# Kernel tuning notes

Hardware: AMD Instinct MI355X
Metric: run time of the kernel (lower is better)

Reference implementation:

```python
import jax, jax.numpy as jnp
import numpy as np

B, N, C = 4, 2048, 768
H = 12
D = C // H  # head_dim = 64
SCALE = D ** -0.5


def setup_inputs() -> dict:
    key = jax.random.key(0)
    ks = jax.random.split(key, 9)
    x_q = jax.random.normal(ks[0], (B, N, C), dtype=jnp.float32)
    x_k = jax.random.normal(ks[1], (B, N, C), dtype=jnp.float32)
    x_v = jax.random.normal(ks[2], (B, N, C), dtype=jnp.float32)
    x_u = jax.random.uniform(ks[3], (B, N, C), dtype=jnp.float32)
    s = C ** -0.5
    Wq = jax.random.normal(ks[4], (C, C), dtype=jnp.float32) * s
    Wk = jax.random.normal(ks[5], (C, C), dtype=jnp.float32) * s
    Wv = jax.random.normal(ks[6], (C, C), dtype=jnp.float32) * s
    Wp = jax.random.normal(ks[7], (C, C), dtype=jnp.float32) * s
    bp = jax.random.normal(ks[8], (C,), dtype=jnp.float32) * 0.01
    return {"x_q": x_q, "x_k": x_k, "x_v": x_v, "x_u": x_u,
            "Wq": Wq, "Wk": Wk, "Wv": Wv, "Wp": Wp, "bp": bp}


def reference(x_q, x_k, x_v, x_u, Wq, Wk, Wv, Wp, bp):
    # Linear projections (torch Linear: y = x @ W.T), split into heads [B,H,N,D]
    def to_heads(x, W):
        y = jnp.einsum('bnc,oc->bno', x, W)
        return y.reshape(B, N, H, D).transpose(0, 2, 1, 3)
    q = to_heads(x_q, Wq) * SCALE
    k = to_heads(x_k, Wk)
    v = to_heads(x_v, Wv)
    # Scores [B,H,N,N]
    attn = jnp.einsum('bhqd,bhkd->bhqk', q, k)
    # Uncertainty map: per-query scalar (mean over channels), broadcast over keys & heads
    uc = jnp.mean(x_u, axis=-1)  # [B,N]
    attn = attn * uc[:, None, :, None]
    attn = jax.nn.softmax(attn, axis=-1)
    out = jnp.einsum('bhqk,bhkd->bhqd', attn, v)
    out = out.transpose(0, 2, 1, 3).reshape(B, N, C)
    return jnp.einsum('bnc,oc->bno', out, Wp) + bp
```

## Files before the change

kernel.cpp:

```cpp
#include <hip/hip_runtime.h>
#include <hip/hip_bf16.h>
#include <cstdint>

#define B_ 4
#define N_ 2048
#define C_ 768
#define H_ 12
#define D_ 64
#define QSCALE 0.18033688011112042f

typedef __bf16 bf16x8 __attribute__((ext_vector_type(8)));
typedef float f32x4 __attribute__((ext_vector_type(4)));

__device__ __forceinline__ unsigned f2bs(float x) {
  unsigned u = __builtin_bit_cast(unsigned, x);
  unsigned r = (u + 0x7fffu + ((u >> 16) & 1u)) >> 16;
  return r;
}

__device__ __forceinline__ bf16x8 ldb8(const unsigned short* p) {
  return __builtin_bit_cast(bf16x8, *(const uint4*)p);
}

__device__ __forceinline__ f32x4 mfma16(bf16x8 a, bf16x8 b, f32x4 c) {
  return __builtin_amdgcn_mfma_f32_16x16x32_bf16(a, b, c, 0, 0, 0);
}

__device__ __forceinline__ void async16(const unsigned short* g, unsigned short* l) {
  __builtin_amdgcn_global_load_lds(
      (const __attribute__((address_space(1))) unsigned int*)g,
      (__attribute__((address_space(3))) unsigned int*)l, 16, 0, 0);
}

__global__ void prep_kernel(
    const float* __restrict__ xq, const float* __restrict__ xk,
    const float* __restrict__ xv, const float* __restrict__ xu,
    const float* __restrict__ Wq, const float* __restrict__ Wk,
    const float* __restrict__ Wv, const float* __restrict__ Wp,
    unsigned short* __restrict__ dxq, unsigned short* __restrict__ dxk,
    unsigned short* __restrict__ dxv,
    unsigned short* __restrict__ dwq, unsigned short* __restrict__ dwk,
    unsigned short* __restrict__ dwv, unsigned short* __restrict__ dwp,
    float* __restrict__ uc) {
  const int id = blockIdx.x;
  if (id < 18432) {
    const float* s = (id < 6144) ? xq : (id < 12288) ? xk : xv;
    unsigned short* d = (id < 6144) ? dxq : (id < 12288) ? dxk : dxv;
    int i = ((id % 6144) * 256 + threadIdx.x) * 4;
    float4 v = *(const float4*)(s + i);
    ushort4 h;
    h.x = (unsigned short)f2bs(v.x); h.y = (unsigned short)f2bs(v.y);
    h.z = (unsigned short)f2bs(v.z); h.w = (unsigned short)f2bs(v.w);
    *(ushort4*)(d + i) = h;
  } else if (id < 20736) {
    int sub = id - 18432;
    int which = sub / 576;
    const float* s = (which == 0) ? Wq : (which == 1) ? Wk : (which == 2) ? Wv : Wp;
    unsigned short* d = (which == 0) ? dwq : (which == 1) ? dwk : (which == 2) ? dwv : dwp;
    int i = ((sub % 576) * 256 + threadIdx.x) * 4;
    float4 v = *(const float4*)(s + i);
    ushort4 h;
    h.x = (unsigned short)f2bs(v.x); h.y = (unsigned short)f2bs(v.y);
    h.z = (unsigned short)f2bs(v.z); h.w = (unsigned short)f2bs(v.w);
    *(ushort4*)(d + i) = h;
  } else {
    int sub = id - 20736;
    int w = threadIdx.x >> 6, lane = threadIdx.x & 63;
    int row = sub * 4 + w;
    const float* p = xu + (size_t)row * C_;
    float s = 0.f;
#pragma unroll
    for (int i = 0; i < 3; ++i) {
      float4 v = *(const float4*)(p + (i * 64 + lane) * 4);
      s += v.x + v.y + v.z + v.w;
    }
#pragma unroll
    for (int off = 1; off < 64; off <<= 1) s += __shfl_xor(s, off);
    if (lane == 0) uc[row] = s * (1.f / 768.f);
  }
}

__device__ __forceinline__ void gemm_mainloop(
    const unsigned short* __restrict__ A, const unsigned short* __restrict__ W,
    int m0, int n0, unsigned short* Al, unsigned short* Bl,
    int tid, int wm, int wn, int quad, int id15, f32x4 (*acc)[4]) {
  const int wb = tid & 192;
  const unsigned short* ap[4];
  const unsigned short* bp[4];
#pragma unroll
  for (int s = 0; s < 4; ++s) {
    int g = s * 256 + tid;
    int row = (g >> 2) & 127;
    int col = ((g >> 9) << 5) | ((g & 3) << 3);
    ap[s] = A + (size_t)(m0 + row) * C_ + col;
    bp[s] = W + (size_t)(n0 + row) * C_ + col;
  }

  for (int kt = 0; kt < C_; kt += 64) {
    __syncthreads();
#pragma unroll
    for (int s = 0; s < 4; ++s) {
      async16(ap[s] + kt, Al + (s * 256 + wb) * 8);
      async16(bp[s] + kt, Bl + (s * 256 + wb) * 8);
    }
    __syncthreads();

#pragma unroll
    for (int kk = 0; kk < 2; ++kk) {
      bf16x8 af[4], bfr[4];
#pragma unroll
      for (int i = 0; i < 4; ++i)
        af[i]  = ldb8(&Al[kk * 4096 + (wm + i * 16 + id15) * 32 + quad * 8]);
#pragma unroll
      for (int j = 0; j < 4; ++j)
        bfr[j] = ldb8(&Bl[kk * 4096 + (wn + j * 16 + id15) * 32 + quad * 8]);
#pragma unroll
      for (int i = 0; i < 4; ++i)
#pragma unroll
        for (int j = 0; j < 4; ++j)
          acc[i][j] = mfma16(af[i], bfr[j], acc[i][j]);
    }
  }
}

#define TSTR 136
__global__ __launch_bounds__(256, 3) void gemm_qkv(
    const unsigned short* __restrict__ xq, const unsigned short* __restrict__ xk,
    const unsigned short* __restrict__ xv,
    const unsigned short* __restrict__ wq, const unsigned short* __restrict__ wk,
    const unsigned short* __restrict__ wv,
    unsigned short* __restrict__ oq, unsigned short* __restrict__ ok,
    unsigned short* __restrict__ ov, const float* __restrict__ uc) {
  __shared__ __align__(16) unsigned short S[128 * TSTR];
  unsigned short* Al = S;
  unsigned short* Bl = S + 8192;
  const int tid = threadIdx.x;
  const int w = tid >> 6, lane = tid & 63, quad = lane >> 4, id15 = lane & 15;
  const int wm = (w >> 1) << 6, wn = (w & 1) << 6;
  const int id = blockIdx.x;
  const int xcd = id & 7, slot = id >> 3;
  const int n0 = (slot % 6) << 7;
  const int gz = xcd * 24 + slot / 6;
  const int z = gz >> 6, m0 = (gz & 63) << 7;

  const unsigned short* A = (z == 0) ? xq : (z == 1) ? xk : xv;
  const unsigned short* W = (z == 0) ? wq : (z == 1) ? wk : wv;

  f32x4 acc[4][4] = {};
  gemm_mainloop(A, W, m0, n0, Al, Bl, tid, wm, wn, quad, id15, acc);

  if (z == 2) {
    __syncthreads();
#pragma unroll
    for (int i = 0; i < 4; ++i)
#pragma unroll
      for (int j = 0; j < 4; ++j) {
        uint2 u;
        u.x = f2bs(acc[i][j][0]) | (f2bs(acc[i][j][1]) << 16);
        u.y = f2bs(acc[i][j][2]) | (f2bs(acc[i][j][3]) << 16);
        *(uint2*)&S[(wn + j * 16 + id15) * TSTR + wm + i * 16 + quad * 4] = u;
      }
    __syncthreads();
    const int b = m0 >> 11, nb = m0 & (N_ - 1);
#pragma unroll
    for (int s = 0; s < 8; ++s) {
      int c = s * 256 + tid;
      int row = c >> 4, o = (c & 15) << 3;
      *(uint4*)(ov + (size_t)(b * C_ + n0 + row) * N_ + nb + o) = *(const uint4*)&S[row * TSTR + o];
    }
    return;
  }

#pragma unroll
  for (int i = 0; i < 4; ++i) {
#pragma unroll
    for (int j = 0; j < 4; ++j) {
#pragma unroll
      for (int r = 0; r < 4; ++r) {
        int gm = m0 + wm + i * 16 + quad * 4 + r;
        int gn = n0 + wn + j * 16 + id15;
        float v = acc[i][j][r];
        if (z == 0) {
          v *= QSCALE * uc[gm];
          oq[(size_t)gm * C_ + gn] = (unsigned short)f2bs(v);
        } else {
          ok[(size_t)gm * C_ + gn] = (unsigned short)f2bs(v);
        }
      }
    }
  }
}

__global__ __launch_bounds__(256, 4) void gemm_out(
    const unsigned short* __restrict__ ao, const unsigned short* __restrict__ wp,
    float* __restrict__ out, const float* __restrict__ bias) {
  __shared__ __align__(16) unsigned short Al[64 * 64];
  __shared__ __align__(16) unsigned short Bl[128 * 64];
  const int tid = threadIdx.x;
  const int w = tid >> 6, lane = tid & 63, quad = lane >> 4, id15 = lane & 15;
  const int wm = (w >> 1) << 5, wn = (w & 1) << 6;
  const int id = blockIdx.x;
  const int xcd = id & 7, slot = id >> 3;
  const int n0 = (slot % 6) << 7;
  const int m0 = (xcd * 16 + slot / 6) << 6;

  const int wb = tid & 192;
  const unsigned short* ap[2];
#pragma unroll
  for (int s = 0; s < 2; ++s) {
    int g = s * 256 + tid;
    int row = (g >> 2) & 63;
    int col = ((g >> 8) << 5) | ((g & 3) << 3);
    ap[s] = ao + (size_t)(m0 + row) * C_ + col;
  }
  const unsigned short* bp[4];
#pragma unroll
  for (int s = 0; s < 4; ++s) {
    int g = s * 256 + tid;
    int row = (g >> 2) & 127;
    int col = ((g >> 9) << 5) | ((g & 3) << 3);
    bp[s] = wp + (size_t)(n0 + row) * C_ + col;
  }

  f32x4 acc[2][4] = {};
  for (int kt = 0; kt < C_; kt += 64) {
    __syncthreads();
#pragma unroll
    for (int s = 0; s < 2; ++s) async16(ap[s] + kt, Al + (s * 256 + wb) * 8);
#pragma unroll
    for (int s = 0; s < 4; ++s) async16(bp[s] + kt, Bl + (s * 256 + wb) * 8);
    __syncthreads();

#pragma unroll
    for (int kk = 0; kk < 2; ++kk) {
      bf16x8 af[2], bfr[4];
#pragma unroll
      for (int i = 0; i < 2; ++i)
        af[i]  = ldb8(&Al[kk * 2048 + (wm + i * 16 + id15) * 32 + quad * 8]);
#pragma unroll
      for (int j = 0; j < 4; ++j)
        bfr[j] = ldb8(&Bl[kk * 4096 + (wn + j * 16 + id15) * 32 + quad * 8]);
#pragma unroll
      for (int i = 0; i < 2; ++i)
#pragma unroll
        for (int j = 0; j < 4; ++j)
          acc[i][j] = mfma16(af[i], bfr[j], acc[i][j]);
    }
  }

#pragma unroll
  for (int i = 0; i < 2; ++i) {
#pragma unroll
    for (int j = 0; j < 4; ++j) {
#pragma unroll
      for (int r = 0; r < 4; ++r) {
        int gm = m0 + wm + i * 16 + quad * 4 + r;
        int gn = n0 + wn + j * 16 + id15;
        out[(size_t)gm * C_ + gn] = acc[i][j][r] + bias[gn];
      }
    }
  }
}

#define KSTR 72
#define PSTR 72
__global__ __launch_bounds__(256, 3) void attn_kernel(
    const unsigned short* __restrict__ Q, const unsigned short* __restrict__ Kk,
    const unsigned short* __restrict__ Vt, unsigned short* __restrict__ O) {
  __shared__ __align__(16) unsigned short Kl[64 * KSTR];
  __shared__ __align__(16) unsigned short Vl[64 * KSTR];
  __shared__ __align__(16) unsigned short Pl[8][16 * PSTR];

  const int tid = threadIdx.x;
  const int w = tid >> 6, lane = tid & 63, quad = lane >> 4, id15 = lane & 15;
  const int id = blockIdx.x;
  const int xcd = id & 7, slot = id >> 3;
  const int bh = xcd * 6 + (slot >> 4);
  const int qt = slot & 15;
  const int b = bh / H_, h = bh % H_;
  const int q0 = qt * 128 + w * 32;

  bf16x8 qf[2][2];
#pragma unroll
  for (int rg = 0; rg < 2; ++rg)
#pragma unroll
    for (int kb = 0; kb < 2; ++kb)
      qf[rg][kb] = ldb8(Q + (size_t)(b * N_ + q0 + rg * 16 + id15) * C_ + h * 64 + kb * 32 + quad * 8);

  const uint4 onesu = {0x3F803F80u, 0x3F803F80u, 0x3F803F80u, 0x3F803F80u};
  const bf16x8 onesf = __builtin_bit_cast(bf16x8, onesu);

  f32x4 oacc[2][4] = {};
  f32x4 lacc[2] = {};

  const size_t kbase = (size_t)(b * N_) * C_ + h * 64;
  const size_t vbase = (size_t)(b * C_ + h * 64) * N_;
  const int srow0 = tid >> 3, srow1 = (256 + tid) >> 3;
  const int sseg0 = (tid & 7) << 3;

  unsigned short* Plw0 = &Pl[w * 2 + 0][0];
  unsigned short* Plw1 = &Pl[w * 2 + 1][0];

  for (int kc = 0; kc < N_; kc += 64) {
    __syncthreads();
    *(uint4*)&Kl[srow0 * KSTR + sseg0] = *(const uint4*)(Kk + kbase + (size_t)(kc + srow0) * C_ + sseg0);
    *(uint4*)&Kl[srow1 * KSTR + sseg0] = *(const uint4*)(Kk + kbase + (size_t)(kc + srow1) * C_ + sseg0);
    *(uint4*)&Vl[srow0 * KSTR + sseg0] = *(const uint4*)(Vt + vbase + (size_t)srow0 * N_ + kc + sseg0);
    *(uint4*)&Vl[srow1 * KSTR + sseg0] = *(const uint4*)(Vt + vbase + (size_t)srow1 * N_ + kc + sseg0);
    __syncthreads();

    f32x4 sA[4], sB[4];
#pragma unroll
    for (int cb = 0; cb < 4; ++cb) {
      f32x4 a = {}, c = {};
#pragma unroll
      for (int kb = 0; kb < 2; ++kb) {
        bf16x8 kf = ldb8(&Kl[(cb * 16 + id15) * KSTR + kb * 32 + quad * 8]);
        a = mfma16(kf, qf[0][kb], a);
        c = mfma16(kf, qf[1][kb], c);
      }
      sA[cb] = a; sB[cb] = c;
    }

#pragma unroll
    for (int rg = 0; rg < 2; ++rg) {
      f32x4* s4 = (rg == 0) ? sA : sB;
      unsigned short* Plw = (rg == 0) ? Plw0 : Plw1;
#pragma unroll
      for (int cb = 0; cb < 4; ++cb) {
        unsigned p0 = __builtin_bit_cast(unsigned, exp2f(s4[cb][0]));
        unsigned p1 = __builtin_bit_cast(unsigned, exp2f(s4[cb][1]));
        unsigned p2 = __builtin_bit_cast(unsigned, exp2f(s4[cb][2]));
        unsigned p3 = __builtin_bit_cast(unsigned, exp2f(s4[cb][3]));
        uint2 u;
        u.x = __builtin_amdgcn_perm(p1, p0, 0x07060302u);
        u.y = __builtin_amdgcn_perm(p3, p2, 0x07060302u);
        *(uint2*)&Plw[id15 * PSTR + cb * 16 + quad * 4] = u;
      }
    }

    bf16x8 pf[2][2];
#pragma unroll
    for (int kb = 0; kb < 2; ++kb) {
      pf[0][kb] = ldb8(&Plw0[id15 * PSTR + kb * 32 + quad * 8]);
      pf[1][kb] = ldb8(&Plw1[id15 * PSTR + kb * 32 + quad * 8]);
    }

#pragma unroll
    for (int kb = 0; kb < 2; ++kb) {
      lacc[0] = mfma16(pf[0][kb], onesf, lacc[0]);
      lacc[1] = mfma16(pf[1][kb], onesf, lacc[1]);
    }
#pragma unroll
    for (int db = 0; db < 4; ++db) {
#pragma unroll
      for (int kb = 0; kb < 2; ++kb) {
        bf16x8 vf = ldb8(&Vl[(db * 16 + id15) * KSTR + kb * 32 + quad * 8]);
        oacc[0][db] = mfma16(pf[0][kb], vf, oacc[0][db]);
        oacc[1][db] = mfma16(pf[1][kb], vf, oacc[1][db]);
      }
    }
  }

#pragma unroll
  for (int rg = 0; rg < 2; ++rg) {
#pragma unroll
    for (int r = 0; r < 4; ++r) {
      float linv = 1.0f / lacc[rg][r];
      int n = q0 + rg * 16 + quad * 4 + r;
#pragma unroll
      for (int db = 0; db < 4; ++db)
        O[(size_t)(b * N_ + n) * C_ + h * 64 + db * 16 + id15] = (unsigned short)f2bs(oacc[rg][db][r] * linv);
    }
  }
}

extern "C" void kernel_launch(void* const* d_in, const int* in_sizes, int n_in,
                              void* d_out, int out_size, void* d_ws, size_t ws_size,
                              hipStream_t stream) {
  const float* x_q = (const float*)d_in[0];
  const float* x_k = (const float*)d_in[1];
  const float* x_v = (const float*)d_in[2];
  const float* x_u = (const float*)d_in[3];
  const float* Wq  = (const float*)d_in[4];
  const float* Wk  = (const float*)d_in[5];
  const float* Wv  = (const float*)d_in[6];
  const float* Wp  = (const float*)d_in[7];
  const float* bp  = (const float*)d_in[8];

  char* ws = (char*)d_ws;
  size_t off = 0;
  auto alloc = [&](size_t bytes) {
    char* p = ws + off;
    off += (bytes + 255) & ~(size_t)255;
    return p;
  };
  unsigned short* wq16 = (unsigned short*)alloc((size_t)C_ * C_ * 2);
  unsigned short* wk16 = (unsigned short*)alloc((size_t)C_ * C_ * 2);
  unsigned short* wv16 = (unsigned short*)alloc((size_t)C_ * C_ * 2);
  unsigned short* wp16 = (unsigned short*)alloc((size_t)C_ * C_ * 2);
  float*          ucp  = (float*)alloc((size_t)B_ * N_ * 4);
  unsigned short* xq16 = (unsigned short*)alloc((size_t)B_ * N_ * C_ * 2);
  unsigned short* xk16 = (unsigned short*)alloc((size_t)B_ * N_ * C_ * 2);
  unsigned short* xv16 = (unsigned short*)alloc((size_t)B_ * N_ * C_ * 2);
  unsigned short* q_s  = (unsigned short*)alloc((size_t)B_ * N_ * C_ * 2);
  unsigned short* k_s  = (unsigned short*)alloc((size_t)B_ * N_ * C_ * 2);
  unsigned short* vT   = (unsigned short*)alloc((size_t)B_ * N_ * C_ * 2);
  unsigned short* ao   = (unsigned short*)alloc((size_t)B_ * N_ * C_ * 2);

  prep_kernel<<<dim3(22784), 256, 0, stream>>>(x_q, x_k, x_v, x_u, Wq, Wk, Wv, Wp,
                                               xq16, xk16, xv16,
                                               wq16, wk16, wv16, wp16, ucp);
  gemm_qkv<<<dim3(1152), 256, 0, stream>>>(xq16, xk16, xv16, wq16, wk16, wv16,
                                           q_s, k_s, vT, ucp);
  attn_kernel<<<dim3(768), 256, 0, stream>>>(q_s, k_s, vT, ao);
  gemm_out<<<dim3(768), 256, 0, stream>>>(ao, wp16, (float*)d_out, bp);
}
```

Baseline: 298.1 us.

## Rework attention to 32x32 MFMA with register-resident P and double-buffered K/V

The attention kernel moves from 16x16x32 to 32x32x16 bf16 MFMA tiles, with one 32-row query tile per wave. The exponentiated scores are repacked with v_cvt_pk_bf16_f32 and ds_bpermute lane shuffles, so they feed the PV MFMA directly instead of going through a per-wave LDS P buffer. K/V chunks are double-buffered in LDS, with the next chunk's global loads issued before the current compute, leaving one barrier per iteration instead of two. This aims to hide global load latency and cut LDS traffic, at the cost of more registers and extra cross-lane permutes.

```diff
diff --git a/kernel.cpp b/kernel.cpp
--- a/kernel.cpp
+++ b/kernel.cpp
@@ -11,6 +11,7 @@
 
 typedef __bf16 bf16x8 __attribute__((ext_vector_type(8)));
 typedef float f32x4 __attribute__((ext_vector_type(4)));
+typedef float f32x16 __attribute__((ext_vector_type(16)));
 
 __device__ __forceinline__ unsigned f2bs(float x) {
   unsigned u = __builtin_bit_cast(unsigned, x);
@@ -24,6 +25,10 @@
 
 __device__ __forceinline__ f32x4 mfma16(bf16x8 a, bf16x8 b, f32x4 c) {
   return __builtin_amdgcn_mfma_f32_16x16x32_bf16(a, b, c, 0, 0, 0);
+}
+
+__device__ __forceinline__ f32x16 mfma32(bf16x8 a, bf16x8 b, f32x16 c) {
+  return __builtin_amdgcn_mfma_f32_32x32x16_bf16(a, b, c, 0, 0, 0);
 }
 
 __device__ __forceinline__ void async16(const unsigned short* g, unsigned short* l) {
@@ -263,16 +268,16 @@
 }
 
 #define KSTR 72
-#define PSTR 72
+#define VOFF (64 * KSTR)
+#define BUFO (2 * 64 * KSTR)
 __global__ __launch_bounds__(256, 3) void attn_kernel(
     const unsigned short* __restrict__ Q, const unsigned short* __restrict__ Kk,
     const unsigned short* __restrict__ Vt, unsigned short* __restrict__ O) {
-  __shared__ __align__(16) unsigned short Kl[64 * KSTR];
-  __shared__ __align__(16) unsigned short Vl[64 * KSTR];
-  __shared__ __align__(16) unsigned short Pl[8][16 * PSTR];
+  __shared__ __align__(16) unsigned short KV[2 * 2 * 64 * KSTR];
 
   const int tid = threadIdx.x;
-  const int w = tid >> 6, lane = tid & 63, quad = lane >> 4, id15 = lane & 15;
+  const int w = tid >> 6, lane = tid & 63;
+  const int i32 = lane & 31, hi = lane >> 5;
   const int id = blockIdx.x;
   const int xcd = id & 7, slot = id >> 3;
   const int bh = xcd * 6 + (slot >> 4);
@@ -280,98 +285,104 @@
   const int b = bh / H_, h = bh % H_;
   const int q0 = qt * 128 + w * 32;
 
-  bf16x8 qf[2][2];
-#pragma unroll
-  for (int rg = 0; rg < 2; ++rg)
-#pragma unroll
-    for (int kb = 0; kb < 2; ++kb)
-      qf[rg][kb] = ldb8(Q + (size_t)(b * N_ + q0 + rg * 16 + id15) * C_ + h * 64 + kb * 32 + quad * 8);
+  bf16x8 qf[4];
+#pragma unroll
+  for (int s = 0; s < 4; ++s)
+    qf[s] = ldb8(Q + (size_t)(b * N_ + q0 + i32) * C_ + h * 64 + s * 16 + hi * 8);
 
   const uint4 onesu = {0x3F803F80u, 0x3F803F80u, 0x3F803F80u, 0x3F803F80u};
   const bf16x8 onesf = __builtin_bit_cast(bf16x8, onesu);
 
-  f32x4 oacc[2][4] = {};
-  f32x4 lacc[2] = {};
+  f32x16 oacc0 = {}, oacc1 = {}, lacc = {};
 
   const size_t kbase = (size_t)(b * N_) * C_ + h * 64;
   const size_t vbase = (size_t)(b * C_ + h * 64) * N_;
-  const int srow0 = tid >> 3, srow1 = (256 + tid) >> 3;
-  const int sseg0 = (tid & 7) << 3;
-
-  unsigned short* Plw0 = &Pl[w * 2 + 0][0];
-  unsigned short* Plw1 = &Pl[w * 2 + 1][0];
-
-  for (int kc = 0; kc < N_; kc += 64) {
-    __syncthreads();
-    *(uint4*)&Kl[srow0 * KSTR + sseg0] = *(const uint4*)(Kk + kbase + (size_t)(kc + srow0) * C_ + sseg0);
-    *(uint4*)&Kl[srow1 * KSTR + sseg0] = *(const uint4*)(Kk + kbase + (size_t)(kc + srow1) * C_ + sseg0);
-    *(uint4*)&Vl[srow0 * KSTR + sseg0] = *(const uint4*)(Vt + vbase + (size_t)srow0 * N_ + kc + sseg0);
-    *(uint4*)&Vl[srow1 * KSTR + sseg0] = *(const uint4*)(Vt + vbase + (size_t)srow1 * N_ + kc + sseg0);
-    __syncthreads();
-
-    f32x4 sA[4], sB[4];
-#pragma unroll
-    for (int cb = 0; cb < 4; ++cb) {
-      f32x4 a = {}, c = {};
-#pragma unroll
-      for (int kb = 0; kb < 2; ++kb) {
-        bf16x8 kf = ldb8(&Kl[(cb * 16 + id15) * KSTR + kb * 32 + quad * 8]);
-        a = mfma16(kf, qf[0][kb], a);
-        c = mfma16(kf, qf[1][kb], c);
-      }
-      sA[cb] = a; sB[cb] = c;
-    }
-
-#pragma unroll
-    for (int rg = 0; rg < 2; ++rg) {
-      f32x4* s4 = (rg == 0) ? sA : sB;
-      unsigned short* Plw = (rg == 0) ? Plw0 : Plw1;
-#pragma unroll
-      for (int cb = 0; cb < 4; ++cb) {
-        unsigned p0 = __builtin_bit_cast(unsigned, exp2f(s4[cb][0]));
-        unsigned p1 = __builtin_bit_cast(unsigned, exp2f(s4[cb][1]));
-        unsigned p2 = __builtin_bit_cast(unsigned, exp2f(s4[cb][2]));
-        unsigned p3 = __builtin_bit_cast(unsigned, exp2f(s4[cb][3]));
-        uint2 u;
-        u.x = __builtin_amdgcn_perm(p1, p0, 0x07060302u);
-        u.y = __builtin_amdgcn_perm(p3, p2, 0x07060302u);
-        *(uint2*)&Plw[id15 * PSTR + cb * 16 + quad * 4] = u;
-      }
-    }
-
-    bf16x8 pf[2][2];
-#pragma unroll
-    for (int kb = 0; kb < 2; ++kb) {
-      pf[0][kb] = ldb8(&Plw0[id15 * PSTR + kb * 32 + quad * 8]);
-      pf[1][kb] = ldb8(&Plw1[id15 * PSTR + kb * 32 + quad * 8]);
-    }
-
-#pragma unroll
-    for (int kb = 0; kb < 2; ++kb) {
-      lacc[0] = mfma16(pf[0][kb], onesf, lacc[0]);
-      lacc[1] = mfma16(pf[1][kb], onesf, lacc[1]);
-    }
-#pragma unroll
-    for (int db = 0; db < 4; ++db) {
-#pragma unroll
-      for (int kb = 0; kb < 2; ++kb) {
-        bf16x8 vf = ldb8(&Vl[(db * 16 + id15) * KSTR + kb * 32 + quad * 8]);
-        oacc[0][db] = mfma16(pf[0][kb], vf, oacc[0][db]);
-        oacc[1][db] = mfma16(pf[1][kb], vf, oacc[1][db]);
-      }
-    }
-  }
-
-#pragma unroll
-  for (int rg = 0; rg < 2; ++rg) {
-#pragma unroll
-    for (int r = 0; r < 4; ++r) {
-      float linv = 1.0f / lacc[rg][r];
-      int n = q0 + rg * 16 + quad * 4 + r;
-#pragma unroll
-      for (int db = 0; db < 4; ++db)
-        O[(size_t)(b * N_ + n) * C_ + h * 64 + db * 16 + id15] = (unsigned short)f2bs(oacc[rg][db][r] * linv);
-    }
+  const int srow0 = tid >> 3, srow1 = 32 + (tid >> 3);
+  const int sseg = (tid & 7) << 3;
+  const int addrLow = i32 << 2;
+  const int addrHigh = addrLow | 128;
+
+  auto compute = [&](const unsigned short* Kc) {
+    const unsigned short* Vc = Kc + VOFF;
+#pragma unroll
+    for (int t = 0; t < 2; ++t) {
+      f32x16 s16 = {};
+#pragma unroll
+      for (int s = 0; s < 4; ++s) {
+        bf16x8 kf = ldb8(Kc + (t * 32 + i32) * KSTR + s * 16 + hi * 8);
+        s16 = mfma32(kf, qf[s], s16);
+      }
+      unsigned Dw[8];
+#pragma unroll
+      for (int j = 0; j < 8; ++j) {
+        float e0 = exp2f(s16[2 * j]);
+        float e1 = exp2f(s16[2 * j + 1]);
+        unsigned d;
+        asm("v_cvt_pk_bf16_f32 %0, %1, %2" : "=v"(d) : "v"(e0), "v"(e1));
+        Dw[j] = d;
+      }
+#pragma unroll
+      for (int sl = 0; sl < 2; ++sl) {
+        const int bb = sl * 4;
+        unsigned L2 = (unsigned)__builtin_amdgcn_ds_bpermute(addrLow, (int)Dw[bb + 2]);
+        unsigned L3 = (unsigned)__builtin_amdgcn_ds_bpermute(addrLow, (int)Dw[bb + 3]);
+        unsigned H0 = (unsigned)__builtin_amdgcn_ds_bpermute(addrHigh, (int)Dw[bb + 0]);
+        unsigned H1 = (unsigned)__builtin_amdgcn_ds_bpermute(addrHigh, (int)Dw[bb + 1]);
+        uint4 u;
+        u.x = hi ? L2 : Dw[bb + 0];
+        u.y = hi ? L3 : Dw[bb + 1];
+        u.z = hi ? Dw[bb + 2] : H0;
+        u.w = hi ? Dw[bb + 3] : H1;
+        bf16x8 pf = __builtin_bit_cast(bf16x8, u);
+        lacc = mfma32(pf, onesf, lacc);
+        bf16x8 v0 = ldb8(Vc + i32 * KSTR + (2 * t + sl) * 16 + hi * 8);
+        bf16x8 v1 = ldb8(Vc + (32 + i32) * KSTR + (2 * t + sl) * 16 + hi * 8);
+        oacc0 = mfma32(pf, v0, oacc0);
+        oacc1 = mfma32(pf, v1, oacc1);
+      }
+    }
+  };
+
+  {
+    uint4 a0 = *(const uint4*)(Kk + kbase + (size_t)srow0 * C_ + sseg);
+    uint4 a1 = *(const uint4*)(Kk + kbase + (size_t)srow1 * C_ + sseg);
+    uint4 c0 = *(const uint4*)(Vt + vbase + (size_t)srow0 * N_ + sseg);
+    uint4 c1 = *(const uint4*)(Vt + vbase + (size_t)srow1 * N_ + sseg);
+    *(uint4*)&KV[srow0 * KSTR + sseg] = a0;
+    *(uint4*)&KV[srow1 * KSTR + sseg] = a1;
+    *(uint4*)&KV[VOFF + srow0 * KSTR + sseg] = c0;
+    *(uint4*)&KV[VOFF + srow1 * KSTR + sseg] = c1;
+  }
+
+  int cur = 0;
+  for (int kc = 0; kc < N_ - 64; kc += 64) {
+    const int kcn = kc + 64;
+    uint4 a0 = *(const uint4*)(Kk + kbase + (size_t)(kcn + srow0) * C_ + sseg);
+    uint4 a1 = *(const uint4*)(Kk + kbase + (size_t)(kcn + srow1) * C_ + sseg);
+    uint4 c0 = *(const uint4*)(Vt + vbase + (size_t)srow0 * N_ + kcn + sseg);
+    uint4 c1 = *(const uint4*)(Vt + vbase + (size_t)srow1 * N_ + kcn + sseg);
+
+    __syncthreads();
+
+    compute(KV + (cur ? BUFO : 0));
+
+    unsigned short* Kn = KV + (cur ? 0 : BUFO);
+    *(uint4*)&Kn[srow0 * KSTR + sseg] = a0;
+    *(uint4*)&Kn[srow1 * KSTR + sseg] = a1;
+    *(uint4*)&Kn[VOFF + srow0 * KSTR + sseg] = c0;
+    *(uint4*)&Kn[VOFF + srow1 * KSTR + sseg] = c1;
+    cur ^= 1;
+  }
+  __syncthreads();
+  compute(KV + (cur ? BUFO : 0));
+
+#pragma unroll
+  for (int r = 0; r < 16; ++r) {
+    float linv = 1.0f / lacc[r];
+    int q = q0 + (r & 3) + 8 * (r >> 2) + 4 * hi;
+    size_t base = (size_t)(b * N_ + q) * C_ + h * 64 + i32;
+    O[base] = (unsigned short)f2bs(oacc0[r] * linv);
+    O[base + 32] = (unsigned short)f2bs(oacc1[r] * linv);
   }
 }
 
```

Result: slower. 310.9 us (+4.3%).
